# Optimization experiments

Measured on AMD Instinct MI355X. Metric: run time of the kernel, lower is better.

Reference implementation:

```python
import jax, jax.numpy as jnp
import numpy as np

B, N, S, C, H = 16, 64, 4096, 768, 1
HEAD_DIM = C // H
SCALE = HEAD_DIM ** -0.5
ASSIGN_EPS = 1.0


def setup_inputs() -> dict:
    key = jax.random.key(0)
    ks = jax.random.split(key, 8)
    w = lambda k: jax.random.normal(k, (C, C), jnp.float32) * 0.02
    return {
        "query": jax.random.normal(ks[0], (B, N, C), jnp.float32),       # group tokens
        "key_tokens": jax.random.normal(ks[1], (B, S, C), jnp.float32),  # sequence tokens
        "Wq": w(ks[2]), "bq": jnp.zeros((C,), jnp.float32),
        "Wk": w(ks[3]), "bk": jnp.zeros((C,), jnp.float32),
        "Wv": w(ks[4]), "bv": jnp.zeros((C,), jnp.float32),
        "Wo": w(ks[5]), "bo": jnp.zeros((C,), jnp.float32),
    }


def reference(query, key_tokens, Wq, bq, Wk, bk, Wv, bv, Wo, bo):
    # AssignAttention forward (hard=True, gumbel=False -> hard_softmax path).
    def split_heads(x):  # [b, t, C] -> [b, h, t, c]
        b, t, _ = x.shape
        return x.reshape(b, t, H, HEAD_DIM).transpose(0, 2, 1, 3)

    q = split_heads(query @ Wq.T + bq)        # [B, H, N, c]
    k = split_heads(key_tokens @ Wk.T + bk)   # [B, H, S, c]
    v = split_heads(key_tokens @ Wv.T + bv)   # [B, H, S, c]

    raw_attn = jnp.einsum('bhnc,bhsc->bhns', q, k) * SCALE  # [B, H, N, S]

    # hard_softmax over the group (query) dim, axis=-2, with straight-through estimator
    y_soft = jax.nn.softmax(raw_attn, axis=-2)
    idx = jnp.argmax(y_soft, axis=-2)                          # [B, H, S]
    y_hard = jnp.swapaxes(jax.nn.one_hot(idx, N, dtype=raw_attn.dtype), -1, -2)  # [B, H, N, S]
    attn = jax.lax.stop_gradient(y_hard - y_soft) + y_soft

    # sum-renormalization over assigned tokens (sum_assign=False)
    attn = attn / (attn.sum(axis=-1, keepdims=True) + ASSIGN_EPS)

    out = jnp.einsum('bhns,bhsc->bhnc', attn, v)  # [B, H, N, c]
    out = out.transpose(0, 2, 1, 3).reshape(B, N, C)
    return out @ Wo.T + bo
```

## Files before the change

### kernel.cpp

```cpp
#include <hip/hip_runtime.h>
#include <hip/hip_bf16.h>

#define BQ 16
#define NG 64
#define SQ 4096
#define CD 768
#define ROWS (BQ*NG)
#define KSP 4

__global__ __launch_bounds__(256)
void transpose64(const float* __restrict__ src, float* __restrict__ dst,
                 int M, int N)
{
    __shared__ float t[64][65];
    const int bx = blockIdx.x * 64;
    const int by = blockIdx.y * 64;
    const int tx = threadIdx.x & 63, tw = threadIdx.x >> 6;
#pragma unroll
    for (int i = 0; i < 16; ++i) {
        const int row = i * 4 + tw;
        t[row][tx] = src[(size_t)(by + row) * N + bx + tx];
    }
    __syncthreads();
#pragma unroll
    for (int i = 0; i < 16; ++i) {
        const int row = i * 4 + tw;
        dst[(size_t)(bx + row) * M + by + tx] = t[tx][row];
    }
}

__global__ __launch_bounds__(256)
void vecmat3(const float* __restrict__ Wq, const float* __restrict__ bk,
             const float* __restrict__ Wk, const float* __restrict__ bq,
             const float* __restrict__ WoT, const float* __restrict__ bv,
             float* __restrict__ uq, float* __restrict__ bqk,
             float* __restrict__ bvo)
{
    __shared__ float red[4][64];
    const float* Mm; const float* v; float* out;
    if (blockIdx.y == 0)      { Mm = Wq;  v = bk; out = uq;  }
    else if (blockIdx.y == 1) { Mm = Wk;  v = bq; out = bqk; }
    else                      { Mm = WoT; v = bv; out = bvo; }
    const int j0 = blockIdx.x * 64;
    const int jl = threadIdx.x & 63;
    const int cs = threadIdx.x >> 6;
    double a = 0.0;
    for (int c = cs; c < CD; c += 4)
        a += (double)Mm[(size_t)c * CD + j0 + jl] * (double)v[c];
    red[cs][jl] = (float)a;
    __syncthreads();
    if (cs == 0) out[j0 + jl] = red[0][jl] + red[1][jl] + red[2][jl] + red[3][jl];
}

__global__ __launch_bounds__(256)
void delta_q(const float* __restrict__ query, const float* __restrict__ uq,
             const float* __restrict__ bq, const float* __restrict__ bk,
             double* __restrict__ delta)
{
    const int r    = blockIdx.x * 4 + (threadIdx.x >> 6);
    const int lane = threadIdx.x & 63;
    double a = 0.0, b = 0.0;
    for (int c = lane; c < CD; c += 64) {
        a += (double)query[(size_t)r * CD + c] * (double)uq[c];
        b += (double)bq[c] * (double)bk[c];
    }
    a += b;
    for (int off = 32; off; off >>= 1) a += __shfl_down(a, off, 64);
    if (lane == 0) delta[r] = a;
}

__device__ __forceinline__
void gemm_core(const float* __restrict__ AT, int lda,
               const float* __restrict__ B,  int ldb,
               float* __restrict__ Pz, int r0, int c0, int k0, int prow0)
{
    __shared__ float As[64][72];
    __shared__ float Bs[64][72];
    const int tid = threadIdx.x;
    const int c4  = tid & 15;
    const int kr  = tid >> 4;
    const int cg  = tid & 15;
    const int rg  = tid >> 4;

    float  acc[4][4]; double acc64[4][4];
#pragma unroll
    for (int i = 0; i < 4; ++i)
#pragma unroll
        for (int j = 0; j < 4; ++j) { acc[i][j] = 0.f; acc64[i][j] = 0.0; }

    for (int ch = 0; ch < 3; ++ch) {
        const int kb = k0 + ch * 64;
        if (ch) __syncthreads();
#pragma unroll
        for (int i = 0; i < 4; ++i) {
            const int row = i * 16 + kr;
            *(float4*)&As[row][4 * c4] = *(const float4*)(AT + (size_t)(kb + row) * lda + r0 + 4 * c4);
            *(float4*)&Bs[row][4 * c4] = *(const float4*)(B  + (size_t)(kb + row) * ldb + c0 + 4 * c4);
        }
        __syncthreads();
#pragma unroll 8
        for (int dd = 0; dd < 64; ++dd) {
            const float4 a = *(const float4*)&As[dd][4 * rg];
            const float4 b = *(const float4*)&Bs[dd][4 * cg];
            const float av[4] = {a.x, a.y, a.z, a.w};
            const float bv[4] = {b.x, b.y, b.z, b.w};
#pragma unroll
            for (int i = 0; i < 4; ++i)
#pragma unroll
                for (int j = 0; j < 4; ++j) acc[i][j] += av[i] * bv[j];
        }
#pragma unroll
        for (int i = 0; i < 4; ++i)
#pragma unroll
            for (int j = 0; j < 4; ++j) { acc64[i][j] += (double)acc[i][j]; acc[i][j] = 0.f; }
    }
#pragma unroll
    for (int i = 0; i < 4; ++i) {
        const int row = prow0 + 4 * rg + i;
        float4 v;
        v.x = (float)acc64[i][0]; v.y = (float)acc64[i][1];
        v.z = (float)acc64[i][2]; v.w = (float)acc64[i][3];
        *(float4*)(Pz + (size_t)row * CD + c0 + 4 * cg) = v;
    }
}

__global__ __launch_bounds__(256)
void gemm_w(const float* __restrict__ Wq, const float* __restrict__ Wk,
            const float* __restrict__ Wv, const float* __restrict__ WoT,
            float* __restrict__ P)
{
    const int by = blockIdx.y;
    float* Pz = P + (size_t)blockIdx.z * (1536 * CD);
    const float* AT; const float* Bp; int r0;
    if (by < 12) { AT = Wq; Bp = Wk;  r0 = by * 64; }
    else         { AT = Wv; Bp = WoT; r0 = (by - 12) * 64; }
    gemm_core(AT, CD, Bp, CD, Pz, r0, blockIdx.x * 64, blockIdx.z * 192, by * 64);
}

__global__ __launch_bounds__(256)
void gemm_d(const float* __restrict__ AT, const float* __restrict__ B,
            float* __restrict__ P)
{
    float* Pz = P + (size_t)blockIdx.z * (ROWS * CD);
    const int r0 = blockIdx.y * 64;
    gemm_core(AT, ROWS, B, CD, Pz, r0, blockIdx.x * 64, blockIdx.z * 192, r0);
}

__global__ __launch_bounds__(256)
void reduce_sk(const float* __restrict__ P, const float* __restrict__ bias,
               const float* __restrict__ bias2, const int* __restrict__ cnt,
               float* __restrict__ out, int M, int mode)
{
    const int e = blockIdx.x * 256 + threadIdx.x;
    if (e >= M * CD) return;
    const size_t MN = (size_t)M * CD;
    double a = 0.0;
#pragma unroll
    for (int z = 0; z < KSP; ++z) a += (double)P[z * MN + e];
    float v = (float)a;
    if (mode == 1) v += bias[e % CD];
    else if (mode == 3) {
        const int r = e / CD;
        const int cv = cnt[r];
        const float invf = 1.f / ((float)cv + 1.f);
        v = v * invf + ((float)cv * invf) * bias2[e % CD] + bias[e % CD];
    }
    out[e] = v;
}

struct ScoreTiles { float gt[64][68]; float kt[64][68]; };
struct ScoreRed   { double bval[64][17]; int bidx[64][17]; };
union  ScoreShared { ScoreTiles t; ScoreRed r; };

__global__ __launch_bounds__(256)
void score_argmax(const float* __restrict__ g, const float* __restrict__ key,
                  const double* __restrict__ delta, int* __restrict__ idxo)
{
    __shared__ alignas(16) ScoreShared sh;
    __shared__ double dl[64];
    const int tid  = threadIdx.x;
    const int b    = blockIdx.y;
    const int s0   = blockIdx.x * 64;
    const int sg   = tid & 15;
    const int ng   = tid >> 4;
    const int lrow = tid >> 4;
    const int c4   = tid & 15;

    if (tid < 64) dl[tid] = delta[b * 64 + tid];

    float  accC[4][4];
    double acc64[4][4];
#pragma unroll
    for (int i = 0; i < 4; ++i)
#pragma unroll
        for (int j = 0; j < 4; ++j) { accC[i][j] = 0.f; acc64[i][j] = 0.0; }

    for (int kc = 0; kc < CD; kc += 64) {
#pragma unroll
        for (int p = 0; p < 4; ++p) {
            const int nrow = p * 16 + lrow;
            const float4 v = *(const float4*)(g + (size_t)(b * 64 + nrow) * CD + kc + 4 * c4);
            sh.t.gt[c4     ][nrow] = v.x;
            sh.t.gt[c4 + 16][nrow] = v.y;
            sh.t.gt[c4 + 32][nrow] = v.z;
            sh.t.gt[c4 + 48][nrow] = v.w;
        }
#pragma unroll
        for (int p = 0; p < 4; ++p) {
            const int srow = p * 16 + lrow;
            const float4 v = *(const float4*)(key + (size_t)(b * SQ + s0 + srow) * CD + kc + 4 * c4);
            const int gs = srow >> 2;
            const int lo = srow & 3;
            const float vv[4] = { v.x, v.y, v.z, v.w };
#pragma unroll
            for (int i = 0; i < 4; ++i) {
                const int dd  = 4 * c4 + i;
                const int row = 16 * i + c4;
                const int col = (((gs + dd) & 15) << 2) + lo;
                sh.t.kt[row][col] = vv[i];
            }
        }
        __syncthreads();
#pragma unroll 4
        for (int dd = 0; dd < 64; ++dd) {
            const int sd = ((dd & 3) << 4) | (dd >> 2);
            const float4 ga = *(const float4*)&sh.t.gt[sd][4 * ng];
            const float4 kf = *(const float4*)&sh.t.kt[sd][((sg + dd) & 15) << 2];
            const float gs_[4] = { ga.x, ga.y, ga.z, ga.w };
            const float ks[4] = { kf.x, kf.y, kf.z, kf.w };
#pragma unroll
            for (int i = 0; i < 4; ++i)
#pragma unroll
                for (int j = 0; j < 4; ++j) accC[i][j] += gs_[i] * ks[j];
        }
        __syncthreads();
#pragma unroll
        for (int i = 0; i < 4; ++i)
#pragma unroll
            for (int j = 0; j < 4; ++j) { acc64[i][j] += (double)accC[i][j]; accC[i][j] = 0.f; }
    }

    double bv[4]; int bn[4];
#pragma unroll
    for (int j = 0; j < 4; ++j) {
        bv[j] = acc64[0][j] + dl[4 * ng + 0]; bn[j] = 4 * ng + 0;
#pragma unroll
        for (int i = 1; i < 4; ++i) {
            const double v = acc64[i][j] + dl[4 * ng + i];
            if (v > bv[j]) { bv[j] = v; bn[j] = 4 * ng + i; }
        }
    }
    __syncthreads();
#pragma unroll
    for (int j = 0; j < 4; ++j) {
        sh.r.bval[4 * sg + j][ng] = bv[j];
        sh.r.bidx[4 * sg + j][ng] = bn[j];
    }
    __syncthreads();
    if (tid < 64) {
        const int s = tid;
        double best = sh.r.bval[s][0]; int bi = sh.r.bidx[s][0];
        for (int k = 1; k < 16; ++k) {
            const double v = sh.r.bval[s][k];
            if (v > best) { best = v; bi = sh.r.bidx[s][k]; }
        }
        idxo[b * SQ + s0 + s] = bi;
    }
}

__global__ __launch_bounds__(256)
void gather_ksum(const float* __restrict__ key, const int* __restrict__ idx,
                 float* __restrict__ Ksum, int* __restrict__ cnt)
{
    __shared__ int slist[SQ];
    __shared__ int scount;
    const int n   = blockIdx.x;
    const int b   = blockIdx.y;
    const int tid = threadIdx.x;
    if (tid == 0) scount = 0;
    __syncthreads();

    const int* ib = idx + b * SQ;
#pragma unroll
    for (int p = 0; p < SQ / 256; ++p) {
        const int s = p * 256 + tid;
        if (ib[s] == n) {
            const int pos = atomicAdd(&scount, 1);
            slist[pos] = s;
        }
    }
    __syncthreads();
    const int m = scount;

    double a0 = 0.0, a1 = 0.0, a2 = 0.0;
    const float* kb = key + (size_t)b * SQ * CD;
    const int c1 = tid + 256, c2 = tid + 512;

    int r = 0;
    for (; r + 4 <= m; r += 4) {
        const float* p0 = kb + (size_t)slist[r]     * CD;
        const float* p1 = kb + (size_t)slist[r + 1] * CD;
        const float* p2 = kb + (size_t)slist[r + 2] * CD;
        const float* p3 = kb + (size_t)slist[r + 3] * CD;
        a0 += (double)p0[tid] + (double)p1[tid] + (double)p2[tid] + (double)p3[tid];
        a1 += (double)p0[c1] + (double)p1[c1] + (double)p2[c1] + (double)p3[c1];
        a2 += (double)p0[c2] + (double)p1[c2] + (double)p2[c2] + (double)p3[c2];
    }
    for (; r < m; ++r) {
        const float* p0 = kb + (size_t)slist[r] * CD;
        a0 += (double)p0[tid]; a1 += (double)p0[c1]; a2 += (double)p0[c2];
    }

    float* out = Ksum + (size_t)(b * 64 + n) * CD;
    out[tid] = (float)a0; out[c1] = (float)a1; out[c2] = (float)a2;
    if (tid == 0) cnt[b * 64 + n] = m;
}

extern "C" void kernel_launch(void* const* d_in, const int* in_sizes, int n_in,
                              void* d_out, int out_size, void* d_ws, size_t ws_size,
                              hipStream_t stream)
{
    const float* query = (const float*)d_in[0];
    const float* key   = (const float*)d_in[1];
    const float* Wq    = (const float*)d_in[2];
    const float* bq    = (const float*)d_in[3];
    const float* Wk    = (const float*)d_in[4];
    const float* bk    = (const float*)d_in[5];
    const float* Wv    = (const float*)d_in[6];
    const float* bv    = (const float*)d_in[7];
    const float* Wo    = (const float*)d_in[8];
    const float* bo    = (const float*)d_in[9];

    char* ws = (char*)d_ws;
    const size_t MB = 1 << 20;
    int*    cnt   = (int*)   (ws + 0);
    double* delta = (double*)(ws + 4096);
    float*  uq    = (float*) (ws + 16384);
    float*  bqk   = (float*) (ws + 19456);
    float*  bvo   = (float*) (ws + 22528);
    int*    idx   = (int*)   (ws + 32768);
    float*  qT    = (float*) (ws + 1 * MB);
    float*  WoT   = (float*) (ws + 4 * MB);
    float*  Wqk   = (float*) (ws + 7 * MB);
    float*  Wvo   = Wqk + 768 * 768;
    float*  g     = (float*) (ws + 12 * MB);
    float*  Ksum  = (float*) (ws + 15 * MB);
    float*  KsumT = (float*) (ws + 18 * MB);
    float*  P     = (float*) (ws + 21 * MB);

    transpose64<<<dim3(12, 12), 256, 0, stream>>>(Wo, WoT, CD, CD);
    transpose64<<<dim3(12, 16), 256, 0, stream>>>(query, qT, ROWS, CD);
    vecmat3<<<dim3(12, 3), 256, 0, stream>>>(Wq, bk, Wk, bq, WoT, bv, uq, bqk, bvo);
    delta_q<<<ROWS / 4, 256, 0, stream>>>(query, uq, bq, bk, delta);
    gemm_w<<<dim3(12, 24, KSP), 256, 0, stream>>>(Wq, Wk, Wv, WoT, P);
    reduce_sk<<<(1536 * CD) / 256, 256, 0, stream>>>(P, nullptr, nullptr, nullptr, Wqk, 1536, 0);
    gemm_d<<<dim3(12, 16, KSP), 256, 0, stream>>>(qT, Wqk, P);
    reduce_sk<<<(ROWS * CD) / 256, 256, 0, stream>>>(P, bqk, nullptr, nullptr, g, ROWS, 1);
    score_argmax<<<dim3(SQ / 64, BQ), 256, 0, stream>>>(g, key, delta, idx);
    gather_ksum<<<dim3(NG, BQ), 256, 0, stream>>>(key, idx, Ksum, cnt);
    transpose64<<<dim3(12, 16), 256, 0, stream>>>(Ksum, KsumT, ROWS, CD);
    gemm_d<<<dim3(12, 16, KSP), 256, 0, stream>>>(KsumT, Wvo, P);
    reduce_sk<<<(ROWS * CD) / 256, 256, 0, stream>>>(P, bo, bvo, cnt, (float*)d_out, ROWS, 3);
}
```

Before: 562.0 us.

## Prefetch next K-chunk into registers in score_argmax and simplify kt layout

The score_argmax GEMM loop now loads the next 64-wide chunk of g and key into registers while computing on the current shared-memory tile, so global loads overlap the FMA work. The swizzled kt store layout is replaced by a plain transposed layout matching gt, and launch bounds now request 4 blocks per CU. The prefetch costs extra registers, and the unswizzled kt layout may bring back LDS bank conflicts on stores.

After: 547.5 us. -2.6%, faster.

```diff
diff --git a/kernel.cpp b/kernel.cpp
--- a/kernel.cpp
+++ b/kernel.cpp
@@ -172,7 +172,7 @@
 struct ScoreRed   { double bval[64][17]; int bidx[64][17]; };
 union  ScoreShared { ScoreTiles t; ScoreRed r; };
 
-__global__ __launch_bounds__(256)
+__global__ __launch_bounds__(256, 4)
 void score_argmax(const float* __restrict__ g, const float* __restrict__ key,
                   const double* __restrict__ delta, int* __restrict__ idxo)
 {
@@ -195,37 +195,50 @@
 #pragma unroll
         for (int j = 0; j < 4; ++j) { accC[i][j] = 0.f; acc64[i][j] = 0.0; }
 
-    for (int kc = 0; kc < CD; kc += 64) {
+    const float* gb = g   + (size_t)(b * 64) * CD;
+    const float* kb = key + (size_t)(b * SQ + s0) * CD;
+
+    float4 rg_[4], rk[4];
+#pragma unroll
+    for (int p = 0; p < 4; ++p) {
+        const int row = p * 16 + lrow;
+        rg_[p] = *(const float4*)(gb + (size_t)row * CD + 4 * c4);
+        rk[p]  = *(const float4*)(kb + (size_t)row * CD + 4 * c4);
+    }
+
+    for (int t = 0; t < 12; ++t) {
+        __syncthreads();
 #pragma unroll
         for (int p = 0; p < 4; ++p) {
             const int nrow = p * 16 + lrow;
-            const float4 v = *(const float4*)(g + (size_t)(b * 64 + nrow) * CD + kc + 4 * c4);
-            sh.t.gt[c4     ][nrow] = v.x;
-            sh.t.gt[c4 + 16][nrow] = v.y;
-            sh.t.gt[c4 + 32][nrow] = v.z;
-            sh.t.gt[c4 + 48][nrow] = v.w;
+            sh.t.gt[c4     ][nrow] = rg_[p].x;
+            sh.t.gt[c4 + 16][nrow] = rg_[p].y;
+            sh.t.gt[c4 + 32][nrow] = rg_[p].z;
+            sh.t.gt[c4 + 48][nrow] = rg_[p].w;
         }
 #pragma unroll
         for (int p = 0; p < 4; ++p) {
             const int srow = p * 16 + lrow;
-            const float4 v = *(const float4*)(key + (size_t)(b * SQ + s0 + srow) * CD + kc + 4 * c4);
-            const int gs = srow >> 2;
-            const int lo = srow & 3;
-            const float vv[4] = { v.x, v.y, v.z, v.w };
-#pragma unroll
-            for (int i = 0; i < 4; ++i) {
-                const int dd  = 4 * c4 + i;
-                const int row = 16 * i + c4;
-                const int col = (((gs + dd) & 15) << 2) + lo;
-                sh.t.kt[row][col] = vv[i];
+            sh.t.kt[c4     ][srow] = rk[p].x;
+            sh.t.kt[c4 + 16][srow] = rk[p].y;
+            sh.t.kt[c4 + 32][srow] = rk[p].z;
+            sh.t.kt[c4 + 48][srow] = rk[p].w;
+        }
+        __syncthreads();
+        if (t < 11) {
+            const int kc = (t + 1) * 64;
+#pragma unroll
+            for (int p = 0; p < 4; ++p) {
+                const int row = p * 16 + lrow;
+                rg_[p] = *(const float4*)(gb + (size_t)row * CD + kc + 4 * c4);
+                rk[p]  = *(const float4*)(kb + (size_t)row * CD + kc + 4 * c4);
             }
         }
-        __syncthreads();
 #pragma unroll 4
         for (int dd = 0; dd < 64; ++dd) {
             const int sd = ((dd & 3) << 4) | (dd >> 2);
             const float4 ga = *(const float4*)&sh.t.gt[sd][4 * ng];
-            const float4 kf = *(const float4*)&sh.t.kt[sd][((sg + dd) & 15) << 2];
+            const float4 kf = *(const float4*)&sh.t.kt[sd][4 * sg];
             const float gs_[4] = { ga.x, ga.y, ga.z, ga.w };
             const float ks[4] = { kf.x, kf.y, kf.z, kf.w };
 #pragma unroll
@@ -233,7 +246,6 @@
 #pragma unroll
                 for (int j = 0; j < 4; ++j) accC[i][j] += gs_[i] * ks[j];
         }
-        __syncthreads();
 #pragma unroll
         for (int i = 0; i < 4; ++i)
 #pragma unroll
```
